# Kernel optimization log

Measured on AMD Instinct MI355X. Metric: run time of the kernel, lower is better.

## Reference

```python
import jax, jax.numpy as jnp
import numpy as np

# Dimensions (see shape_source)
B, D, Q, M = 2, 1024, 1024, 1024
K = Q + M                      # klen = mlen + qlen
N_HEAD, D_HEAD = 16, 64        # n_head * d_head == d_model
D_INNER = 4096
LOCAL_SIZE = 1000              # Attention: self.local_size or 1000
EPS = 1e-5                     # F.layer_norm default eps


def setup_inputs() -> dict:
    key = jax.random.key(0)
    ks = jax.random.split(key, 12)
    z = jax.random.normal(ks[0], (B, D, Q), jnp.float32)
    z_hist = jax.random.normal(ks[1], (B, D, M), jnp.float32)
    u = jax.random.normal(ks[2], (B, 3 * N_HEAD * D_HEAD, K), jnp.float32) * 0.1
    # sinusoidal relative position embedding (PositionalEmbedding), positions K-1..0
    inv_freq = 1.0 / (10000.0 ** (jnp.arange(0, D, 2, dtype=jnp.float32) / D))
    pos_seq = jnp.arange(K - 1, -1, -1, dtype=jnp.float32)
    sinusoid = inv_freq[:, None] * pos_seq[None, :]  # (D/2, K)
    pos_emb = jnp.concatenate([jnp.sin(sinusoid), jnp.cos(sinusoid)], axis=0)[None]  # (1, D, K)
    s = 0.02
    W_qkv = jax.random.normal(ks[3], (3 * N_HEAD * D_HEAD, D), jnp.float32) * s
    W_r = jax.random.normal(ks[4], (N_HEAD * D_HEAD, D), jnp.float32) * s
    r_w_bias = jax.random.uniform(ks[5], (N_HEAD, D_HEAD), jnp.float32, -0.05, 0.05)
    r_r_bias = jax.random.uniform(ks[6], (N_HEAD, D_HEAD), jnp.float32, -0.05, 0.05)
    W_o = jax.random.normal(ks[7], (D, N_HEAD * D_HEAD), jnp.float32) * s
    b_o = jnp.zeros((D,), jnp.float32)
    W_ff1 = jax.random.normal(ks[8], (D_INNER, D), jnp.float32) * s
    b_ff1 = jnp.zeros((D_INNER,), jnp.float32)
    W_ff2 = jax.random.normal(ks[9], (D, D_INNER), jnp.float32) * s
    b_ff2 = jnp.zeros((D,), jnp.float32)
    return dict(z=z, z_hist=z_hist, u=u, pos_emb=pos_emb, W_qkv=W_qkv, W_r=W_r,
                r_w_bias=r_w_bias, r_r_bias=r_r_bias, W_o=W_o, b_o=b_o,
                W_ff1=W_ff1, b_ff1=b_ff1, W_ff2=W_ff2, b_ff2=b_ff2)


def _ln(x, axis):
    # F.layer_norm without affine params
    mu = jnp.mean(x, axis=axis, keepdims=True)
    var = jnp.var(x, axis=axis, keepdims=True)
    return (x - mu) / jnp.sqrt(var + EPS)


def _rel_shift(x):
    # Transformer-XL relative shift: pad left on key dim, reinterpret, drop row.
    b, n, q, k = x.shape
    x = jnp.pad(x, ((0, 0), (0, 0), (0, 0), (1, 0)))
    x = x.reshape(b, n, k + 1, q)
    return x[:, :, 1:, :].reshape(b, n, q, k)


def reference(z, z_hist, u, pos_emb, W_qkv, W_r, r_w_bias, r_r_bias, W_o, b_o,
              W_ff1, b_ff1, W_ff2, b_ff2):
    scale = 1.0 / (D_HEAD ** 0.5)
    # ---- Attention (post-LN, Conv1d kernel=1 == pointwise matmul) ----
    cat = jnp.concatenate([z_hist, z], axis=2)                 # (B, D, K)
    w_heads = jnp.einsum('od,bdk->bok', W_qkv, cat) + u        # (B, 3*n*dh, K)
    q_h, k_h, v_h = jnp.split(w_heads, 3, axis=1)
    q_h = q_h[:, :, -Q:].reshape(B, N_HEAD, D_HEAD, Q)
    k_h = k_h.reshape(B, N_HEAD, D_HEAD, K)
    v_h = v_h.reshape(B, N_HEAD, D_HEAD, K)
    r_k = jnp.einsum('od,dk->ok', W_r, pos_emb[0]).reshape(N_HEAD, D_HEAD, K)
    AC = jnp.einsum('bndi,bndj->bnij', q_h + r_w_bias[:, :, None], k_h)
    BD = _rel_shift(jnp.einsum('bndi,ndj->bnij', q_h + r_r_bias[:, :, None], r_k))
    score = (AC + BD) * scale                                  # (B, n, Q, K)
    causal = jnp.triu(jnp.ones((Q, K), bool), k=1 + M)         # future tokens
    local = jnp.tril(jnp.ones((Q, K), bool), k=M - LOCAL_SIZE)  # beyond local window
    mask = causal | local
    score = jnp.where(mask[None, None], -jnp.inf, score)
    prob = jax.nn.softmax(score, axis=-1)
    attn_vec = jnp.einsum('bnij,bndj->bndi', prob, v_h).reshape(B, N_HEAD * D_HEAD, Q)
    attn_out = jnp.einsum('od,bdq->boq', W_o, attn_vec) + b_o[None, :, None]
    out = _ln(attn_out + z, axis=1)                            # LN over d_model (dim=1)
    # ---- FFN (operates token-major) ----
    h = out.transpose(0, 2, 1)                                 # (B, Q, D)
    ff = jnp.maximum(h @ W_ff1.T + b_ff1, 0.0) @ W_ff2.T + b_ff2
    y = _ln(ff + h, axis=-1)
    return y.transpose(0, 2, 1)                                # (B, D, Q)
```

## Files before the change

### kernel.cpp

```cpp
#include <hip/hip_runtime.h>

#define D_MODEL 1024
#define QLEN 1024

typedef __bf16 bf16x8 __attribute__((ext_vector_type(8)));
typedef __bf16 bf16x4 __attribute__((ext_vector_type(4)));
typedef float f32x4 __attribute__((ext_vector_type(4)));

__device__ __forceinline__ void gload16(const void* g, void* l) {
    __builtin_amdgcn_global_load_lds(
        (const __attribute__((address_space(1))) void*)g,
        (__attribute__((address_space(3))) void*)l, 16, 0, 0);
}

__device__ __forceinline__ void gemm_core8(
    __bf16* __restrict__ smA, __bf16* __restrict__ smB,
    const __bf16* __restrict__ A, const __bf16* __restrict__ Bt,
    float* __restrict__ C, __bf16* __restrict__ Cb,
    const float* __restrict__ U, const __bf16* __restrict__ Ub,
    const float* __restrict__ bias,
    int K, int lda, int ldb, int ldC, int ldU, int relu, int m0, int n0)
{
    const int t = threadIdx.x;
    const int lane = t & 63, w = t >> 6;
    const int l15 = lane & 15, lg = lane >> 4;
    const int wm = w >> 2, wn = w & 3;
    const int srow = lane >> 3, cpr = lane & 7;
    const int NK = K >> 6;
    const int SZ = 128 * 64;

    #define STAGE(buf, kt)                                                                   \
    {                                                                                        \
        int k0s = (kt) * 64;                                                                 \
        _Pragma("unroll")                                                                    \
        for (int i = 0; i < 2; ++i) {                                                        \
            int r = w * 16 + i * 8 + srow;                                                   \
            int c = cpr ^ (r & 7);                                                           \
            gload16(&A[(long long)(m0 + r) * lda + k0s + c * 8],                             \
                    &smA[(buf) * SZ + (w * 16 + i * 8) * 64]);                               \
            gload16(&Bt[(long long)(n0 + r) * ldb + k0s + c * 8],                            \
                    &smB[(buf) * SZ + (w * 16 + i * 8) * 64]);                               \
        }                                                                                    \
    }

    f32x4 acc[4][2] = {};
    STAGE(0, 0);

    for (int kt = 0; kt < NK; ++kt) {
        const int cb = kt & 1;
        if (kt + 1 < NK) {
            STAGE(cb ^ 1, kt + 1);
            asm volatile("s_waitcnt vmcnt(4)" ::: "memory");
        } else {
            asm volatile("s_waitcnt vmcnt(0)" ::: "memory");
        }
        __builtin_amdgcn_sched_barrier(0);
        __builtin_amdgcn_s_barrier();

        #pragma unroll
        for (int kk = 0; kk < 2; ++kk) {
            bf16x8 bfr[2];
            #pragma unroll
            for (int nt = 0; nt < 2; ++nt) {
                int nr = wn * 32 + nt * 16 + l15;
                bfr[nt] = *(const bf16x8*)&smB[cb * SZ + nr * 64 + (((kk * 4 + lg) ^ (nr & 7)) * 8)];
            }
            #pragma unroll
            for (int mt = 0; mt < 4; ++mt) {
                int mr = wm * 64 + mt * 16 + l15;
                bf16x8 afr = *(const bf16x8*)&smA[cb * SZ + mr * 64 + (((kk * 4 + lg) ^ (mr & 7)) * 8)];
                #pragma unroll
                for (int nt = 0; nt < 2; ++nt)
                    acc[mt][nt] = __builtin_amdgcn_mfma_f32_16x16x32_bf16(afr, bfr[nt], acc[mt][nt], 0, 0, 0);
            }
        }
        asm volatile("s_waitcnt lgkmcnt(0)" ::: "memory");
        __builtin_amdgcn_sched_barrier(0);
        __builtin_amdgcn_s_barrier();
    }
    #undef STAGE

    #pragma unroll
    for (int mt = 0; mt < 4; ++mt) {
        #pragma unroll
        for (int nt = 0; nt < 2; ++nt) {
            #pragma unroll
            for (int rg = 0; rg < 4; ++rg) {
                int m = m0 + wm * 64 + mt * 16 + lg * 4 + rg;
                int n = n0 + wn * 32 + nt * 16 + l15;
                float v = acc[mt][nt][rg];
                if (U)    v += U[(long long)m * ldU + n];
                if (Ub)   v += (float)Ub[(long long)m * ldU + n];
                if (bias) v += bias[n];
                if (relu) v = fmaxf(v, 0.0f);
                if (Cb) Cb[(long long)m * ldC + n] = (__bf16)v;
                else    C [(long long)m * ldC + n] = v;
            }
        }
    }
}

template<int KS>
__global__ __launch_bounds__(512) void gemm_bf16_k(
    const __bf16* __restrict__ A, const __bf16* __restrict__ Bt,
    float* __restrict__ C, __bf16* __restrict__ Cb,
    const float* __restrict__ U, const __bf16* __restrict__ Ub,
    const float* __restrict__ bias,
    int K, int lda, int ldb, int ldC, int ldU, int relu,
    long long sA, long long sB, long long sC, long long sU, long long sSplit)
{
    __shared__ __bf16 SM[32768];
    const int bz = blockIdx.z;
    int yb = blockIdx.y;
    int half = 0;
    if (KS) { half = yb & 1; yb >>= 1; }
    A  += (long long)bz * sA + (long long)half * K;
    Bt += (long long)bz * sB + (long long)half * K;
    if (C)  C  += (long long)bz * sC + (long long)half * sSplit;
    if (Cb) Cb += (long long)bz * sC;
    if (U)  U  += (long long)bz * sU;
    if (Ub) Ub += (long long)bz * sU;
    if (KS && half) { bias = nullptr; U = nullptr; Ub = nullptr; }
    gemm_core8(SM, SM + 16384, A, Bt, C, Cb, U, Ub, bias,
               K, lda, ldb, ldC, ldU, relu, yb * 128, blockIdx.x * 128);
}

__global__ __launch_bounds__(512) void gemm_fused3(
    const __bf16* __restrict__ cat_t, const __bf16* __restrict__ Wqkvb,
    __bf16* __restrict__ qkT, const __bf16* __restrict__ uqkT,
    __bf16* __restrict__ wh_v, const float* __restrict__ uv,
    const __bf16* __restrict__ pos_t, const __bf16* __restrict__ Wrb,
    __bf16* __restrict__ rkT)
{
    __shared__ __bf16 SM[32768];
    int bid = blockIdx.x;
    if (bid < 512) {
        int zz = bid >> 8, rem = bid & 255, y = rem >> 4, x = rem & 15;
        gemm_core8(SM, SM + 16384,
                   cat_t + (long long)zz * 2097152, Wqkvb,
                   nullptr, qkT + (long long)zz * 4194304,
                   nullptr, uqkT + (long long)zz * 4194304, nullptr,
                   1024, 1024, 1024, 2048, 2048, 0, y * 128, x * 128);
    } else if (bid < 768) {
        int l = bid - 512, zz = l >> 7, rem = l & 127, y = rem >> 4, x = rem & 15;
        gemm_core8(SM, SM + 16384,
                   Wqkvb + 2048 * 1024, cat_t + (long long)zz * 2097152,
                   nullptr, wh_v + (long long)zz * 2097152,
                   uv + (long long)zz * 6291456, nullptr, nullptr,
                   1024, 1024, 1024, 2048, 2048, 0, y * 128, x * 128);
    } else {
        int l = bid - 768, y = l >> 3, x = l & 7;
        gemm_core8(SM, SM + 16384,
                   pos_t + 960 * 1024, Wrb,
                   nullptr, rkT, nullptr, nullptr, nullptr,
                   1024, 1024, 1024, 1024, 0, 0, y * 128, x * 128);
    }
}

__global__ __launch_bounds__(256) void prep_all(
    const float* __restrict__ Wqkv, __bf16* __restrict__ Wqkvb,
    const float* __restrict__ Wr,   __bf16* __restrict__ Wrb,
    const float* __restrict__ Wo,   __bf16* __restrict__ Wob,
    const float* __restrict__ Wff1, __bf16* __restrict__ Wff1b,
    const float* __restrict__ Wff2, __bf16* __restrict__ Wff2b,
    const float* __restrict__ zh, const float* __restrict__ z, __bf16* __restrict__ cat_t,
    const float* __restrict__ pos, __bf16* __restrict__ pos_t,
    const float* __restrict__ u, __bf16* __restrict__ uqkT)
{
    __shared__ float ts[32][33];
    int bid = blockIdx.x;
    const int t = threadIdx.x;
    if (bid < 13312) {
        long long i = ((long long)bid * 256 + t) * 4;
        const float* s; __bf16* dd;
        if (i < 3145728)                    { s = Wqkv + i; dd = Wqkvb + i; }
        else if ((i -= 3145728) < 1048576)  { s = Wr + i;   dd = Wrb + i; }
        else if ((i -= 1048576) < 1048576)  { s = Wo + i;   dd = Wob + i; }
        else if ((i -= 1048576) < 4194304)  { s = Wff1 + i; dd = Wff1b + i; }
        else { i -= 4194304;                  s = Wff2 + i; dd = Wff2b + i; }
        float4 v = *(const float4*)s;
        bf16x4 o = { (__bf16)v.x, (__bf16)v.y, (__bf16)v.z, (__bf16)v.w };
        *(bf16x4*)dd = o;
        return;
    }
    bid -= 13312;
    const float* S; __bf16* D; int R, Cc, bx, by;
    if (bid < 2048) {
        int zz = bid >> 10, r2 = bid & 1023;
        S = zh + (long long)zz * 1048576; D = cat_t + (long long)zz * 2097152;
        R = 1024; Cc = 1024; bx = r2 & 31; by = r2 >> 5;
    } else if (bid < 4096) {
        int l = bid - 2048; int zz = l >> 10, r2 = l & 1023;
        S = z + (long long)zz * 1048576; D = cat_t + 1048576 + (long long)zz * 2097152;
        R = 1024; Cc = 1024; bx = r2 & 31; by = r2 >> 5;
    } else if (bid < 6144) {
        int l = bid - 4096;
        S = pos; D = pos_t; R = 1024; Cc = 2048; bx = l & 63; by = l >> 6;
    } else if (bid < 14336) {
        int l = bid - 6144; int zz = l >> 12, r2 = l & 4095;
        S = u + (long long)zz * 6291456; D = uqkT + (long long)zz * 4194304;
        R = 2048; Cc = 2048; bx = r2 & 63; by = r2 >> 6;
    } else {
        int l = bid - 14336;
        int i = (l * 256 + t) * 4;
        bf16x4 zv = { (__bf16)0.f, (__bf16)0.f, (__bf16)0.f, (__bf16)0.f };
        *(bf16x4*)&pos_t[2048 * 1024 + i] = zv;
        return;
    }
    int r0 = by * 32, c0 = bx * 32;
    int tr = t >> 5, tc = t & 31;
    #pragma unroll
    for (int p = 0; p < 4; ++p)
        ts[tr + p * 8][tc] = S[(long long)(r0 + tr + p * 8) * Cc + c0 + tc];
    __syncthreads();
    #pragma unroll
    for (int p = 0; p < 4; ++p)
        D[(long long)(c0 + tr + p * 8) * R + r0 + tc] = (__bf16)ts[tc][tr + p * 8];
}

__global__ __launch_bounds__(256) void attn_mfma(
    const __bf16* __restrict__ QKT, const __bf16* __restrict__ WHV,
    const __bf16* __restrict__ RKT,
    const float* __restrict__ rwb, const float* __restrict__ rrb,
    __bf16* __restrict__ AVt)
{
    __shared__ __bf16 SM[38144];
    __bf16* KT0 = SM;
    __bf16* KT1 = SM + 4096;
    __bf16* VS0 = SM + 8192;
    __bf16* VS1 = SM + 12288;
    __bf16* RT  = SM + 16384;
    __bf16* PS  = SM + 28672;
    __bf16* BT  = SM + 32768;

    const int d = blockIdx.x;
    const int xcd = d & 7, idx = d >> 3;
    const int qt = idx & 15;
    const int gq = xcd + 8 * (idx >> 4);
    const int b = gq >> 4, n = gq & 15;
    const int i0 = qt * 64;

    const int t = threadIdx.x;
    const int lane = t & 63, w = t >> 6;
    const int l15 = lane & 15, lg = lane >> 4;
    const int fco = n * 64;

    const __bf16* qkb = QKT + (long long)b * (2048 * 2048);
    const __bf16* vb  = WHV + (long long)b * (1024 * 2048) + (long long)fco * 2048;
    __bf16* BTw = BT + w * 1344;

    #pragma unroll
    for (int pp = 0; pp < 2; ++pp) {
        int cid = pp * 256 + t;
        int q = cid >> 3, s = cid & 7, c = s ^ (q & 7);
        bf16x8 qv = *(const bf16x8*)&qkb[(long long)(1024 + i0 + q) * 2048 + fco + c * 8];
        bf16x8 ow, orr;
        #pragma unroll
        for (int e = 0; e < 8; ++e) {
            float qf = (float)qv[e];
            ow[e]  = (__bf16)(qf + rwb[fco + c * 8 + e]);
            orr[e] = (__bf16)(qf + rrb[fco + c * 8 + e]);
        }
        *(bf16x8*)&PS[q * 64 + s * 8] = ow;
        *(bf16x8*)&VS0[q * 64 + s * 8] = orr;
    }
    __syncthreads();

    #define LDF(buf, row, ch) (*(const bf16x8*)&(buf)[(row) * 64 + ((((ch) ^ ((row) & 7))) * 8)])

    const int mrow = w * 16 + l15;
    bf16x8 qw0 = LDF(PS, mrow, lg), qw1 = LDF(PS, mrow, lg + 4);
    bf16x8 qr0 = LDF(VS0, mrow, lg), qr1 = LDF(VS0, mrow, lg + 4);
    asm volatile("s_waitcnt lgkmcnt(0)" ::: "memory");
    __builtin_amdgcn_sched_barrier(0);
    __builtin_amdgcn_s_barrier();

    #pragma unroll
    for (int pp = 0; pp < 2; ++pp) {
        int cid = pp * 256 + t;
        int r = cid >> 3, s = cid & 7, c = s ^ (r & 7);
        gload16(&qkb[(long long)(i0 + r) * 2048 + 1024 + fco + c * 8], &KT0[(pp * 32 + w * 8) * 64]);
        gload16(&vb[(long long)r * 2048 + i0 + c * 8], &VS0[(pp * 32 + w * 8) * 64]);
    }
    #pragma unroll
    for (int pp = 0; pp < 6; ++pp) {
        int cid = pp * 256 + t;
        int r = cid >> 3, s = cid & 7, c = s ^ (r & 7);
        gload16(&RKT[(long long)r * 1024 + fco + c * 8], &RT[(pp * 32 + w * 8) * 64]);
    }
    asm volatile("s_waitcnt vmcnt(0)" ::: "memory");
    __builtin_amdgcn_sched_barrier(0);
    __builtin_amdgcn_s_barrier();

    const bf16x8 ones = { (__bf16)1.f, (__bf16)1.f, (__bf16)1.f, (__bf16)1.f,
                          (__bf16)1.f, (__bf16)1.f, (__bf16)1.f, (__bf16)1.f };

    f32x4 O0 = {}, O1 = {}, O2 = {}, O3 = {};
    float rm[4] = {-1e30f, -1e30f, -1e30f, -1e30f};
    float rl[4] = {0.f, 0.f, 0.f, 0.f};
    int cur = 0;

    for (int kt = 0; kt <= 16; ++kt) {
        __bf16* KTc = cur ? KT1 : KT0;
        __bf16* VSc = cur ? VS1 : VS0;
        __bf16* KTn = cur ? KT0 : KT1;
        __bf16* VSn = cur ? VS0 : VS1;
        const int rbase = (kt % 3) * 64;

        if (kt < 16) {
            int j0n = i0 + (kt + 1) * 64;
            #pragma unroll
            for (int pp = 0; pp < 2; ++pp) {
                int cid = pp * 256 + t;
                int r = cid >> 3, s = cid & 7, c = s ^ (r & 7);
                gload16(&qkb[(long long)(j0n + r) * 2048 + 1024 + fco + c * 8], &KTn[(pp * 32 + w * 8) * 64]);
                gload16(&vb[(long long)r * 2048 + j0n + c * 8], &VSn[(pp * 32 + w * 8) * 64]);
            }
            int rb = kt * 64 + 128;
            int lb = ((kt + 2) % 3) * 64;
            #pragma unroll
            for (int pp = 0; pp < 2; ++pp) {
                int cid = pp * 256 + t;
                int r = cid >> 3, s = cid & 7, c = s ^ (r & 7);
                gload16(&RKT[(long long)(rb + r) * 1024 + fco + c * 8], &RT[(lb + pp * 32 + w * 8) * 64]);
            }
        }
        __builtin_amdgcn_sched_barrier(0);

        __builtin_amdgcn_s_setprio(1);
        #pragma unroll
        for (int k5 = 0; k5 < 5; ++k5) {
            int pr = (3 - w + k5) * 16 + l15;
            int lr = rbase + pr; if (lr >= 192) lr -= 192;
            const __bf16* rrow = &RT[lr * 64];
            f32x4 cc = {};
            cc = __builtin_amdgcn_mfma_f32_16x16x32_bf16(qr0, *(const bf16x8*)&rrow[((lg ^ (pr & 7)) * 8)], cc, 0, 0, 0);
            cc = __builtin_amdgcn_mfma_f32_16x16x32_bf16(qr1, *(const bf16x8*)&rrow[(((lg + 4) ^ (pr & 7)) * 8)], cc, 0, 0, 0);
            #pragma unroll
            for (int rg = 0; rg < 4; ++rg)
                BTw[(lg * 4 + rg) * 84 + k5 * 16 + l15] = (__bf16)cc[rg];
        }
        __builtin_amdgcn_s_setprio(0);

        f32x4 cc4[4];
        __builtin_amdgcn_s_setprio(1);
        #pragma unroll
        for (int nt = 0; nt < 4; ++nt) {
            int jr = nt * 16 + l15;
            f32x4 cc = {};
            cc = __builtin_amdgcn_mfma_f32_16x16x32_bf16(qw0, LDF(KTc, jr, lg), cc, 0, 0, 0);
            cc = __builtin_amdgcn_mfma_f32_16x16x32_bf16(qw1, LDF(KTc, jr, lg + 4), cc, 0, 0, 0);
            cc4[nt] = cc;
        }
        __builtin_amdgcn_s_setprio(0);

        const bool bnd = (kt < 2) | (kt == 16);
        float sv[4][4];
        if (!bnd) {
            #pragma unroll
            for (int nt = 0; nt < 4; ++nt) {
                int jr = nt * 16 + l15;
                #pragma unroll
                for (int rg = 0; rg < 4; ++rg) {
                    int r4 = lg * 4 + rg;
                    sv[nt][rg] = (cc4[nt][rg] + (float)BTw[r4 * 84 + jr - r4 + 15]) * 0.125f;
                }
            }
        } else {
            #pragma unroll
            for (int nt = 0; nt < 4; ++nt) {
                int jr = nt * 16 + l15;
                #pragma unroll
                for (int rg = 0; rg < 4; ++rg) {
                    int r4 = lg * 4 + rg;
                    int dji = jr - (w * 16 + r4);
                    float s = (cc4[nt][rg] + (float)BTw[r4 * 84 + jr - r4 + 15]) * 0.125f;
                    bool valid = (kt == 0) ? (dji >= 25)
                               : (kt == 1) ? (dji >= -39)
                               : (dji <= 0);
                    sv[nt][rg] = valid ? s : -1e30f;
                }
            }
        }

        float lmax[4];
        bool need = false;
        #pragma unroll
        for (int rg = 0; rg < 4; ++rg) {
            lmax[rg] = fmaxf(fmaxf(sv[0][rg], sv[1][rg]), fmaxf(sv[2][rg], sv[3][rg]));
            need = need || (lmax[rg] > rm[rg] + 8.0f);
        }
        if (__any(need)) {
            #pragma unroll
            for (int rg = 0; rg < 4; ++rg) {
                float m = lmax[rg];
                m = fmaxf(m, __shfl_xor(m, 1, 16));
                m = fmaxf(m, __shfl_xor(m, 2, 16));
                m = fmaxf(m, __shfl_xor(m, 4, 16));
                m = fmaxf(m, __shfl_xor(m, 8, 16));
                float nm = fmaxf(rm[rg], m);
                float fac = __expf(rm[rg] - nm);
                rm[rg] = nm;
                rl[rg] *= fac;
                O0[rg] *= fac; O1[rg] *= fac; O2[rg] *= fac; O3[rg] *= fac;
            }
        }

        if (!bnd) {
            #pragma unroll
            for (int nt = 0; nt < 4; ++nt) {
                int jc = nt * 16 + l15;
                #pragma unroll
                for (int rg = 0; rg < 4; ++rg) {
                    float p = __expf(sv[nt][rg] - rm[rg]);
                    int row = w * 16 + lg * 4 + rg;
                    PS[row * 64 + (((jc >> 3) ^ (row & 7)) * 8) + (jc & 7)] = (__bf16)p;
                }
            }
        } else {
            #pragma unroll
            for (int nt = 0; nt < 4; ++nt) {
                int jc = nt * 16 + l15;
                #pragma unroll
                for (int rg = 0; rg < 4; ++rg) {
                    float p = (sv[nt][rg] > -1e29f) ? __expf(sv[nt][rg] - rm[rg]) : 0.0f;
                    int row = w * 16 + lg * 4 + rg;
                    PS[row * 64 + (((jc >> 3) ^ (row & 7)) * 8) + (jc & 7)] = (__bf16)p;
                }
            }
        }

        bf16x8 pa0 = LDF(PS, mrow, lg), pa1 = LDF(PS, mrow, lg + 4);
        f32x4 Os = {};
        __builtin_amdgcn_s_setprio(1);
        Os = __builtin_amdgcn_mfma_f32_16x16x32_bf16(pa0, ones, Os, 0, 0, 0);
        Os = __builtin_amdgcn_mfma_f32_16x16x32_bf16(pa1, ones, Os, 0, 0, 0);
        O0 = __builtin_amdgcn_mfma_f32_16x16x32_bf16(pa0, LDF(VSc,  0 + l15, lg),     O0, 0, 0, 0);
        O0 = __builtin_amdgcn_mfma_f32_16x16x32_bf16(pa1, LDF(VSc,  0 + l15, lg + 4), O0, 0, 0, 0);
        O1 = __builtin_amdgcn_mfma_f32_16x16x32_bf16(pa0, LDF(VSc, 16 + l15, lg),     O1, 0, 0, 0);
        O1 = __builtin_amdgcn_mfma_f32_16x16x32_bf16(pa1, LDF(VSc, 16 + l15, lg + 4), O1, 0, 0, 0);
        O2 = __builtin_amdgcn_mfma_f32_16x16x32_bf16(pa0, LDF(VSc, 32 + l15, lg),     O2, 0, 0, 0);
        O2 = __builtin_amdgcn_mfma_f32_16x16x32_bf16(pa1, LDF(VSc, 32 + l15, lg + 4), O2, 0, 0, 0);
        O3 = __builtin_amdgcn_mfma_f32_16x16x32_bf16(pa0, LDF(VSc, 48 + l15, lg),     O3, 0, 0, 0);
        O3 = __builtin_amdgcn_mfma_f32_16x16x32_bf16(pa1, LDF(VSc, 48 + l15, lg + 4), O3, 0, 0, 0);
        __builtin_amdgcn_s_setprio(0);
        #pragma unroll
        for (int rg = 0; rg < 4; ++rg) rl[rg] += Os[rg];

        asm volatile("s_waitcnt vmcnt(0)" ::: "memory");
        __builtin_amdgcn_sched_barrier(0);
        __builtin_amdgcn_s_barrier();
        cur ^= 1;
    }

    #pragma unroll
    for (int rg = 0; rg < 4; ++rg) {
        float inv = 1.0f / rl[rg];
        int q = i0 + w * 16 + lg * 4 + rg;
        long long base = ((long long)b * 1024 + q) * 1024 + fco;
        AVt[base +  0 + l15] = (__bf16)(O0[rg] * inv);
        AVt[base + 16 + l15] = (__bf16)(O1[rg] * inv);
        AVt[base + 32 + l15] = (__bf16)(O2[rg] * inv);
        AVt[base + 48 + l15] = (__bf16)(O3[rg] * inv);
    }
    #undef LDF
}

__global__ __launch_bounds__(256) void ln1_kernel(
    const float* __restrict__ AO, const float* __restrict__ AO2,
    const float* __restrict__ bo, const __bf16* __restrict__ CatT,
    __bf16* __restrict__ Hb)
{
    int i = blockIdx.x, b = blockIdx.y, t = threadIdx.x;
    __shared__ float xs[D_MODEL];
    __shared__ float red[256];
    __shared__ float smu, srstd;
    long long tb = ((long long)b * 1024 + i) * 1024;
    long long zb = ((long long)b * 2048 + 1024 + i) * 1024;

    float lsum = 0.0f;
    for (int dd = t; dd < D_MODEL; dd += 256) {
        float v = AO[tb + dd] + AO2[tb + dd] + bo[dd] + (float)CatT[zb + dd];
        xs[dd] = v;
        lsum += v;
    }
    red[t] = lsum; __syncthreads();
    for (int s2 = 128; s2 > 0; s2 >>= 1) { if (t < s2) red[t] += red[t + s2]; __syncthreads(); }
    if (t == 0) smu = red[0] * (1.0f / D_MODEL);
    __syncthreads();
    float mu = smu;

    float lq = 0.0f;
    for (int dd = t; dd < D_MODEL; dd += 256) { float c = xs[dd] - mu; lq += c * c; }
    red[t] = lq; __syncthreads();
    for (int s2 = 128; s2 > 0; s2 >>= 1) { if (t < s2) red[t] += red[t + s2]; __syncthreads(); }
    if (t == 0) srstd = rsqrtf(red[0] * (1.0f / D_MODEL) + 1e-5f);
    __syncthreads();
    float rstd = srstd;

    for (int dd = t; dd < D_MODEL; dd += 256)
        Hb[tb + dd] = (__bf16)((xs[dd] - mu) * rstd);
}

__global__ __launch_bounds__(256) void ln2_stats(
    const float* __restrict__ F2a, const float* __restrict__ F2b,
    const __bf16* __restrict__ Hb, float2* __restrict__ st)
{
    int i = blockIdx.x, b = blockIdx.y, t = threadIdx.x;
    __shared__ float rs[256], rq[256];
    long long tb = ((long long)b * 1024 + i) * 1024;

    float s = 0.f, q = 0.f;
    for (int dd = t; dd < D_MODEL; dd += 256) {
        float v = F2a[tb + dd] + F2b[tb + dd] + (float)Hb[tb + dd];
        s += v; q += v * v;
    }
    rs[t] = s; rq[t] = q; __syncthreads();
    for (int s2 = 128; s2 > 0; s2 >>= 1) {
        if (t < s2) { rs[t] += rs[t + s2]; rq[t] += rq[t + s2]; }
        __syncthreads();
    }
    if (t == 0) {
        float mu = rs[0] * (1.0f / D_MODEL);
        float var = rq[0] * (1.0f / D_MODEL) - mu * mu;
        st[(long long)b * 1024 + i] = make_float2(mu, rsqrtf(var + 1e-5f));
    }
}

__global__ __launch_bounds__(256) void ln2_write(
    const float* __restrict__ F2a, const float* __restrict__ F2b,
    const __bf16* __restrict__ Hb, const float2* __restrict__ st,
    float* __restrict__ OUT)
{
    __shared__ float ts[32][33];
    int f0 = blockIdx.x * 32, i0 = blockIdx.y * 32, b = blockIdx.z;
    int tr = threadIdx.x >> 5, tc = threadIdx.x & 31;
    #pragma unroll
    for (int p = 0; p < 4; ++p) {
        int tok = i0 + tr + p * 8;
        long long tb = ((long long)b * 1024 + tok) * 1024;
        float2 s = st[(long long)b * 1024 + tok];
        float v = F2a[tb + f0 + tc] + F2b[tb + f0 + tc] + (float)Hb[tb + f0 + tc];
        ts[tr + p * 8][tc] = (v - s.x) * s.y;
    }
    __syncthreads();
    #pragma unroll
    for (int p = 0; p < 4; ++p)
        OUT[((long long)b * 1024 + f0 + tr + p * 8) * 1024 + i0 + tc] = ts[tc][tr + p * 8];
}

extern "C" void kernel_launch(void* const* d_in, const int* in_sizes, int n_in,
                              void* d_out, int out_size, void* d_ws, size_t ws_size,
                              hipStream_t stream) {
    const float* z    = (const float*)d_in[0];
    const float* zh   = (const float*)d_in[1];
    const float* u    = (const float*)d_in[2];
    const float* pos  = (const float*)d_in[3];
    const float* Wqkv = (const float*)d_in[4];
    const float* Wr   = (const float*)d_in[5];
    const float* rwb  = (const float*)d_in[6];
    const float* rrb  = (const float*)d_in[7];
    const float* Wo   = (const float*)d_in[8];
    const float* bo   = (const float*)d_in[9];
    const float* Wff1 = (const float*)d_in[10];
    const float* bff1 = (const float*)d_in[11];
    const float* Wff2 = (const float*)d_in[12];
    const float* bff2 = (const float*)d_in[13];
    float* out = (float*)d_out;
    float* ws  = (float*)d_ws;

    __bf16* cat_t = (__bf16*)ws;
    __bf16* pos_t = (__bf16*)(ws + 2097152);
    __bf16* Wqkvb = (__bf16*)(ws + 3178496);
    __bf16* Wrb   = (__bf16*)(ws + 4751360);
    __bf16* Wob   = (__bf16*)(ws + 5275648);
    __bf16* Wff1b = (__bf16*)(ws + 5799936);
    __bf16* Wff2b = (__bf16*)(ws + 7897088);
    __bf16* uqkT  = (__bf16*)(ws + 9994240);
    __bf16* qkT   = (__bf16*)(ws + 14188544);
    __bf16* wh_v  = (__bf16*)(ws + 18382848);
    __bf16* rkT   = (__bf16*)(ws + 20480000);
    __bf16* av_t  = (__bf16*)(ws + 21069824);
    float*  ao    = ws + 22118400;
    __bf16* h_bf  = (__bf16*)(ws + 26312704);
    float2* st2   = (float2*)(ws + 27361280);
    __bf16* f1b   = (__bf16*)(ws + 14188544);
    float*  f2    = ws + 9994240;

    prep_all<<<27712, 256, 0, stream>>>(
        Wqkv, Wqkvb, Wr, Wrb, Wo, Wob, Wff1, Wff1b, Wff2, Wff2b,
        zh, z, cat_t, pos, pos_t, u, uqkT);

    gemm_fused3<<<840, 512, 0, stream>>>(
        cat_t, Wqkvb, qkT, uqkT, wh_v, u + 4194304, pos_t, Wrb, rkT);

    attn_mfma<<<512, 256, 0, stream>>>(qkT, wh_v, rkT, rwb, rrb, av_t);

    gemm_bf16_k<1><<<dim3(8, 32, 1), 512, 0, stream>>>(
        av_t, Wob, ao, nullptr, nullptr, nullptr, nullptr,
        512, 1024, 1024, 1024, 0, 0, 0LL, 0LL, 0LL, 0LL, 2097152LL);
    ln1_kernel<<<dim3(1024, 2), 256, 0, stream>>>(ao, ao + 2097152, bo, cat_t, h_bf);
    gemm_bf16_k<0><<<dim3(32, 16, 1), 512, 0, stream>>>(
        h_bf, Wff1b, nullptr, f1b, nullptr, nullptr, bff1,
        1024, 1024, 1024, 4096, 0, 1, 0LL, 0LL, 0LL, 0LL, 0LL);
    gemm_bf16_k<1><<<dim3(8, 32, 1), 512, 0, stream>>>(
        f1b, Wff2b, f2, nullptr, nullptr, nullptr, bff2,
        2048, 4096, 4096, 1024, 0, 0, 0LL, 0LL, 0LL, 0LL, 2097152LL);
    ln2_stats<<<dim3(1024, 2), 256, 0, stream>>>(f2, f2 + 2097152, h_bf, st2);
    ln2_write<<<dim3(32, 32, 2), 256, 0, stream>>>(f2, f2 + 2097152, h_bf, st2, out);
}
```

Before: 218.1 us.

## Split attention over keys with merge kernel, 4-way split-K GEMMs, XCD block remap

The attention kernel now runs as two halves over the key tiles. Each half writes unnormalized outputs plus its running max and sum, and a new merge kernel combines them flash-decoding style, doubling the number of blocks. The W_o and FF2 GEMMs move from 2-way to 4-way split-K, with the LayerNorm kernels summing four partial buffers. The fused QKV GEMM remaps block ids across XCDs. The intent is better occupancy and load balance across CUs, at the cost of extra fp32 partial traffic, an extra launch, and workspace aliasing that must not overlap live buffers.

```diff
diff --git a/kernel.cpp b/kernel.cpp
--- a/kernel.cpp
+++ b/kernel.cpp
@@ -100,29 +100,27 @@
     }
 }
 
-template<int KS>
+template<int KSPLIT>
 __global__ __launch_bounds__(512) void gemm_bf16_k(
     const __bf16* __restrict__ A, const __bf16* __restrict__ Bt,
-    float* __restrict__ C, __bf16* __restrict__ Cb,
+    float* __restrict__ C0, float* __restrict__ C1,
+    float* __restrict__ C2, float* __restrict__ C3,
+    __bf16* __restrict__ Cb,
     const float* __restrict__ U, const __bf16* __restrict__ Ub,
     const float* __restrict__ bias,
-    int K, int lda, int ldb, int ldC, int ldU, int relu,
-    long long sA, long long sB, long long sC, long long sU, long long sSplit)
+    int K, int lda, int ldb, int ldC, int ldU, int relu)
 {
     __shared__ __bf16 SM[32768];
-    const int bz = blockIdx.z;
     int yb = blockIdx.y;
     int half = 0;
-    if (KS) { half = yb & 1; yb >>= 1; }
-    A  += (long long)bz * sA + (long long)half * K;
-    Bt += (long long)bz * sB + (long long)half * K;
-    if (C)  C  += (long long)bz * sC + (long long)half * sSplit;
-    if (Cb) Cb += (long long)bz * sC;
-    if (U)  U  += (long long)bz * sU;
-    if (Ub) Ub += (long long)bz * sU;
-    if (KS && half) { bias = nullptr; U = nullptr; Ub = nullptr; }
+    if (KSPLIT > 1) { half = yb & (KSPLIT - 1); yb /= KSPLIT; }
+    const int Keff = K / KSPLIT;
+    A  += (long long)half * Keff;
+    Bt += (long long)half * Keff;
+    float* C = (half == 0) ? C0 : (half == 1) ? C1 : (half == 2) ? C2 : C3;
+    if (half) { bias = nullptr; U = nullptr; Ub = nullptr; }
     gemm_core8(SM, SM + 16384, A, Bt, C, Cb, U, Ub, bias,
-               K, lda, ldb, ldC, ldU, relu, yb * 128, blockIdx.x * 128);
+               Keff, lda, ldb, ldC, ldU, relu, yb * 128, blockIdx.x * 128);
 }
 
 __global__ __launch_bounds__(512) void gemm_fused3(
@@ -133,7 +131,8 @@
     __bf16* __restrict__ rkT)
 {
     __shared__ __bf16 SM[32768];
-    int bid = blockIdx.x;
+    int hw = blockIdx.x;
+    int bid = (hw & 7) * 105 + (hw >> 3);
     if (bid < 512) {
         int zz = bid >> 8, rem = bid & 255, y = rem >> 4, x = rem & 15;
         gemm_core8(SM, SM + 16384,
@@ -222,7 +221,7 @@
     const __bf16* __restrict__ QKT, const __bf16* __restrict__ WHV,
     const __bf16* __restrict__ RKT,
     const float* __restrict__ rwb, const float* __restrict__ rrb,
-    __bf16* __restrict__ AVt)
+    float* __restrict__ AO, float2* __restrict__ ML)
 {
     __shared__ __bf16 SM[38144];
     __bf16* KT0 = SM;
@@ -235,10 +234,15 @@
 
     const int d = blockIdx.x;
     const int xcd = d & 7, idx = d >> 3;
-    const int qt = idx & 15;
-    const int gq = xcd + 8 * (idx >> 4);
+    const int sk = idx & 1;
+    const int idx2 = idx >> 1;
+    const int qt = idx2 & 15;
+    const int gq = xcd + 8 * (idx2 >> 4);
     const int b = gq >> 4, n = gq & 15;
     const int i0 = qt * 64;
+    const int bn = b * 16 + n;
+    const int kt0 = sk ? 9 : 0;
+    const int ktend = sk ? 16 : 8;
 
     const int t = threadIdx.x;
     const int lane = t & 63, w = t >> 6;
@@ -275,18 +279,25 @@
     __builtin_amdgcn_sched_barrier(0);
     __builtin_amdgcn_s_barrier();
 
-    #pragma unroll
-    for (int pp = 0; pp < 2; ++pp) {
-        int cid = pp * 256 + t;
-        int r = cid >> 3, s = cid & 7, c = s ^ (r & 7);
-        gload16(&qkb[(long long)(i0 + r) * 2048 + 1024 + fco + c * 8], &KT0[(pp * 32 + w * 8) * 64]);
-        gload16(&vb[(long long)r * 2048 + i0 + c * 8], &VS0[(pp * 32 + w * 8) * 64]);
-    }
-    #pragma unroll
-    for (int pp = 0; pp < 6; ++pp) {
-        int cid = pp * 256 + t;
-        int r = cid >> 3, s = cid & 7, c = s ^ (r & 7);
-        gload16(&RKT[(long long)r * 1024 + fco + c * 8], &RT[(pp * 32 + w * 8) * 64]);
+    {
+        int j00 = i0 + kt0 * 64;
+        #pragma unroll
+        for (int pp = 0; pp < 2; ++pp) {
+            int cid = pp * 256 + t;
+            int r = cid >> 3, s = cid & 7, c = s ^ (r & 7);
+            gload16(&qkb[(long long)(j00 + r) * 2048 + 1024 + fco + c * 8], &KT0[(pp * 32 + w * 8) * 64]);
+            gload16(&vb[(long long)r * 2048 + j00 + c * 8], &VS0[(pp * 32 + w * 8) * 64]);
+        }
+        #pragma unroll
+        for (int pp = 0; pp < 6; ++pp) {
+            int r0w = pp * 32 + w * 8;
+            int pc = r0w >> 6;
+            int sl = ((kt0 + pc) % 3) * 64 + (r0w & 63);
+            int cid = pp * 256 + t;
+            int rrel = cid >> 3, s = cid & 7;
+            int c = s ^ (rrel & 7);
+            gload16(&RKT[(long long)(kt0 * 64 + rrel) * 1024 + fco + c * 8], &RT[sl * 64]);
+        }
     }
     asm volatile("s_waitcnt vmcnt(0)" ::: "memory");
     __builtin_amdgcn_sched_barrier(0);
@@ -300,14 +311,14 @@
     float rl[4] = {0.f, 0.f, 0.f, 0.f};
     int cur = 0;
 
-    for (int kt = 0; kt <= 16; ++kt) {
+    for (int kt = kt0; kt <= ktend; ++kt) {
         __bf16* KTc = cur ? KT1 : KT0;
         __bf16* VSc = cur ? VS1 : VS0;
         __bf16* KTn = cur ? KT0 : KT1;
         __bf16* VSn = cur ? VS0 : VS1;
         const int rbase = (kt % 3) * 64;
 
-        if (kt < 16) {
+        if (kt < ktend) {
             int j0n = i0 + (kt + 1) * 64;
             #pragma unroll
             for (int pp = 0; pp < 2; ++pp) {
@@ -455,19 +466,53 @@
 
     #pragma unroll
     for (int rg = 0; rg < 4; ++rg) {
-        float inv = 1.0f / rl[rg];
-        int q = i0 + w * 16 + lg * 4 + rg;
-        long long base = ((long long)b * 1024 + q) * 1024 + fco;
-        AVt[base +  0 + l15] = (__bf16)(O0[rg] * inv);
-        AVt[base + 16 + l15] = (__bf16)(O1[rg] * inv);
-        AVt[base + 32 + l15] = (__bf16)(O2[rg] * inv);
-        AVt[base + 48 + l15] = (__bf16)(O3[rg] * inv);
+        int row = w * 16 + lg * 4 + rg;
+        long long ob = ((((long long)sk * 32 + bn) * 16 + qt) * 64 + row) * 64;
+        AO[ob +  0 + l15] = O0[rg];
+        AO[ob + 16 + l15] = O1[rg];
+        AO[ob + 32 + l15] = O2[rg];
+        AO[ob + 48 + l15] = O3[rg];
+        if (l15 == 0)
+            ML[(((long long)sk * 32 + bn) * 16 + qt) * 64 + row] = make_float2(rm[rg], rl[rg]);
     }
     #undef LDF
 }
 
+__global__ __launch_bounds__(256) void attn_merge(
+    const float* __restrict__ AO, const float2* __restrict__ ML,
+    __bf16* __restrict__ AVt)
+{
+    const int bid = blockIdx.x;
+    const int bn = bid >> 4, qt = bid & 15;
+    const int b = bn >> 4, n = bn & 15;
+    const int t = threadIdx.x;
+    const int r = t >> 2, seg = t & 3;
+
+    long long mli = ((long long)bn * 16 + qt) * 64 + r;
+    float2 ml0 = ML[mli];
+    float2 ml1 = ML[(long long)32 * 16 * 64 + mli];
+    float M = fmaxf(ml0.x, ml1.x);
+    float e0 = __expf(ml0.x - M), e1 = __expf(ml1.x - M);
+    float inv = 1.0f / (ml0.y * e0 + ml1.y * e1);
+    float s0 = e0 * inv, s1 = e1 * inv;
+
+    long long ob = (((long long)bn * 16 + qt) * 64 + r) * 64 + seg * 16;
+    long long o1 = ob + (long long)32 * 16 * 64 * 64;
+    long long av = ((long long)b * 1024 + qt * 64 + r) * 1024 + n * 64 + seg * 16;
+    #pragma unroll
+    for (int k = 0; k < 4; ++k) {
+        f32x4 v0 = *(const f32x4*)&AO[ob + k * 4];
+        f32x4 v1 = *(const f32x4*)&AO[o1 + k * 4];
+        bf16x4 o;
+        #pragma unroll
+        for (int e = 0; e < 4; ++e) o[e] = (__bf16)(v0[e] * s0 + v1[e] * s1);
+        *(bf16x4*)&AVt[av + k * 4] = o;
+    }
+}
+
 __global__ __launch_bounds__(256) void ln1_kernel(
-    const float* __restrict__ AO, const float* __restrict__ AO2,
+    const float* __restrict__ A0, const float* __restrict__ A1,
+    const float* __restrict__ A2, const float* __restrict__ A3,
     const float* __restrict__ bo, const __bf16* __restrict__ CatT,
     __bf16* __restrict__ Hb)
 {
@@ -480,7 +525,8 @@
 
     float lsum = 0.0f;
     for (int dd = t; dd < D_MODEL; dd += 256) {
-        float v = AO[tb + dd] + AO2[tb + dd] + bo[dd] + (float)CatT[zb + dd];
+        float v = A0[tb + dd] + A1[tb + dd] + A2[tb + dd] + A3[tb + dd]
+                + bo[dd] + (float)CatT[zb + dd];
         xs[dd] = v;
         lsum += v;
     }
@@ -503,7 +549,8 @@
 }
 
 __global__ __launch_bounds__(256) void ln2_stats(
-    const float* __restrict__ F2a, const float* __restrict__ F2b,
+    const float* __restrict__ F0, const float* __restrict__ F1,
+    const float* __restrict__ F2p, const float* __restrict__ F3,
     const __bf16* __restrict__ Hb, float2* __restrict__ st)
 {
     int i = blockIdx.x, b = blockIdx.y, t = threadIdx.x;
@@ -512,7 +559,7 @@
 
     float s = 0.f, q = 0.f;
     for (int dd = t; dd < D_MODEL; dd += 256) {
-        float v = F2a[tb + dd] + F2b[tb + dd] + (float)Hb[tb + dd];
+        float v = F0[tb + dd] + F1[tb + dd] + F2p[tb + dd] + F3[tb + dd] + (float)Hb[tb + dd];
         s += v; q += v * v;
     }
     rs[t] = s; rq[t] = q; __syncthreads();
@@ -528,7 +575,8 @@
 }
 
 __global__ __launch_bounds__(256) void ln2_write(
-    const float* __restrict__ F2a, const float* __restrict__ F2b,
+    const float* __restrict__ F0, const float* __restrict__ F1,
+    const float* __restrict__ F2p, const float* __restrict__ F3,
     const __bf16* __restrict__ Hb, const float2* __restrict__ st,
     float* __restrict__ OUT)
 {
@@ -540,7 +588,8 @@
         int tok = i0 + tr + p * 8;
         long long tb = ((long long)b * 1024 + tok) * 1024;
         float2 s = st[(long long)b * 1024 + tok];
-        float v = F2a[tb + f0 + tc] + F2b[tb + f0 + tc] + (float)Hb[tb + f0 + tc];
+        float v = F0[tb + f0 + tc] + F1[tb + f0 + tc] + F2p[tb + f0 + tc] + F3[tb + f0 + tc]
+                + (float)Hb[tb + f0 + tc];
         ts[tr + p * 8][tc] = (v - s.x) * s.y;
     }
     __syncthreads();
@@ -581,11 +630,19 @@
     __bf16* wh_v  = (__bf16*)(ws + 18382848);
     __bf16* rkT   = (__bf16*)(ws + 20480000);
     __bf16* av_t  = (__bf16*)(ws + 21069824);
-    float*  ao    = ws + 22118400;
+    float*  ao0   = ws + 22118400;
+    float*  ao1   = ws + 24215552;
+    float*  ao2   = ws + 14188544;
+    float*  ao3   = ws + 16285696;
     __bf16* h_bf  = (__bf16*)(ws + 26312704);
     float2* st2   = (float2*)(ws + 27361280);
+    float2* ml    = (float2*)(ws + 27365376);
+    float*  attnO = ws + 9994240;
     __bf16* f1b   = (__bf16*)(ws + 14188544);
-    float*  f2    = ws + 9994240;
+    float*  f20   = ws + 9994240;
+    float*  f21   = ws + 12091392;
+    float*  f22   = ws + 18382848;
+    float*  f23   = ws + 22118400;
 
     prep_all<<<27712, 256, 0, stream>>>(
         Wqkv, Wqkvb, Wr, Wrb, Wo, Wob, Wff1, Wff1b, Wff2, Wff2b,
@@ -594,18 +651,19 @@
     gemm_fused3<<<840, 512, 0, stream>>>(
         cat_t, Wqkvb, qkT, uqkT, wh_v, u + 4194304, pos_t, Wrb, rkT);
 
-    attn_mfma<<<512, 256, 0, stream>>>(qkT, wh_v, rkT, rwb, rrb, av_t);
-
-    gemm_bf16_k<1><<<dim3(8, 32, 1), 512, 0, stream>>>(
-        av_t, Wob, ao, nullptr, nullptr, nullptr, nullptr,
-        512, 1024, 1024, 1024, 0, 0, 0LL, 0LL, 0LL, 0LL, 2097152LL);
-    ln1_kernel<<<dim3(1024, 2), 256, 0, stream>>>(ao, ao + 2097152, bo, cat_t, h_bf);
-    gemm_bf16_k<0><<<dim3(32, 16, 1), 512, 0, stream>>>(
-        h_bf, Wff1b, nullptr, f1b, nullptr, nullptr, bff1,
-        1024, 1024, 1024, 4096, 0, 1, 0LL, 0LL, 0LL, 0LL, 0LL);
-    gemm_bf16_k<1><<<dim3(8, 32, 1), 512, 0, stream>>>(
-        f1b, Wff2b, f2, nullptr, nullptr, nullptr, bff2,
-        2048, 4096, 4096, 1024, 0, 0, 0LL, 0LL, 0LL, 0LL, 2097152LL);
-    ln2_stats<<<dim3(1024, 2), 256, 0, stream>>>(f2, f2 + 2097152, h_bf, st2);
-    ln2_write<<<dim3(32, 32, 2), 256, 0, stream>>>(f2, f2 + 2097152, h_bf, st2, out);
-}
+    attn_mfma<<<1024, 256, 0, stream>>>(qkT, wh_v, rkT, rwb, rrb, attnO, ml);
+    attn_merge<<<512, 256, 0, stream>>>(attnO, ml, av_t);
+
+    gemm_bf16_k<4><<<dim3(8, 64, 1), 512, 0, stream>>>(
+        av_t, Wob, ao0, ao1, ao2, ao3, nullptr, nullptr, nullptr, nullptr,
+        1024, 1024, 1024, 1024, 0, 0);
+    ln1_kernel<<<dim3(1024, 2), 256, 0, stream>>>(ao0, ao1, ao2, ao3, bo, cat_t, h_bf);
+    gemm_bf16_k<1><<<dim3(32, 16, 1), 512, 0, stream>>>(
+        h_bf, Wff1b, nullptr, nullptr, nullptr, nullptr, f1b, nullptr, nullptr, bff1,
+        1024, 1024, 1024, 4096, 0, 1);
+    gemm_bf16_k<4><<<dim3(8, 64, 1), 512, 0, stream>>>(
+        f1b, Wff2b, f20, f21, f22, f23, nullptr, nullptr, nullptr, bff2,
+        4096, 4096, 4096, 1024, 0, 0);
+    ln2_stats<<<dim3(1024, 2), 256, 0, stream>>>(f20, f21, f22, f23, h_bf, st2);
+    ln2_write<<<dim3(32, 32, 2), 256, 0, stream>>>(f20, f21, f22, f23, h_bf, st2, out);
+}
```

New measurement: 247.5 us. +13.5%, slower.
